# Kernel optimization log

Measured on AMD Instinct MI355X. Metric: run time of the kernel, lower is better.

The kernel has to match this reference:

```python
import jax, jax.numpy as jnp
import numpy as np

B, L, C, K, S = 8, 4096, 512, 5, 8


def setup_inputs() -> dict:
    key = jax.random.key(0)
    ks = jax.random.split(key, 5)
    x = jax.random.normal(ks[0], (B, L, C), dtype=jnp.float32)
    # contiguous random partition of [0, L) into S segments per batch row
    rng = np.random.default_rng(0)
    cuts = np.sort(rng.integers(1, L, size=(B, S - 1)), axis=1)
    starts = np.concatenate([np.zeros((B, 1), np.int64), cuts.astype(np.int64)], axis=1)
    ends = np.concatenate([cuts.astype(np.int64), np.full((B, 1), L, np.int64)], axis=1)
    segment_boundaries = jnp.asarray(np.stack([starts, ends], axis=-1))  # [B,S,2]
    fan = 1.0 / np.sqrt(K)
    w_dw = jax.random.normal(ks[1], (C, K), dtype=jnp.float32) * fan
    b_dw = jax.random.normal(ks[2], (C,), dtype=jnp.float32) * 0.01
    w_pw = jax.random.normal(ks[3], (C, C), dtype=jnp.float32) * (1.0 / np.sqrt(C))
    b_pw = jax.random.normal(ks[4], (C,), dtype=jnp.float32) * 0.01
    return {"x": x, "segment_boundaries": segment_boundaries,
            "w_dw": w_dw, "b_dw": b_dw, "w_pw": w_pw, "b_pw": b_pw}


def reference(x, segment_boundaries, w_dw, b_dw, w_pw, b_pw):
    # x: [B,L,C]; segment_boundaries: [B,S,2]; w_dw: [C,K]; w_pw: [C_out,C_in]
    Bx, Lx, Cx = x.shape
    Kx = w_dw.shape[1]
    starts = segment_boundaries[..., 0]  # [B,S]
    ends = segment_boundaries[..., 1]    # [B,S]
    pos = jnp.arange(Lx)
    in_seg = (pos[None, None, :] >= starts[..., None]) & (pos[None, None, :] < ends[..., None])  # [B,S,L]
    covered = in_seg.any(axis=1)                                  # [B,L]
    seg_id = jnp.where(covered, jnp.argmax(in_seg, axis=1), -1)   # [B,L]

    # causal depthwise conv with left zero-pad per segment (no cross-segment leakage)
    acc = jnp.zeros_like(x)
    for d in range(Kx):  # d = how far back we look; tap index = K-1-d
        if d == 0:
            x_s, id_s = x, seg_id
        else:
            x_s = jnp.pad(x, ((0, 0), (d, 0), (0, 0)))[:, :Lx]
            id_s = jnp.pad(seg_id, ((0, 0), (d, 0)), constant_values=-2)[:, :Lx]
        m = ((seg_id == id_s) & covered).astype(x.dtype)          # [B,L]
        acc = acc + w_dw[:, Kx - 1 - d] * x_s * m[..., None]
    dw = acc + b_dw                                               # [B,L,C]
    pw = jnp.einsum('blc,dc->bld', dw, w_pw) + b_pw               # pointwise 1x1 conv
    return pw * covered[..., None].astype(x.dtype)                # zeros outside segments
```

## Files before the change

kernel.cpp:

```cpp
#include <hip/hip_runtime.h>
#include <hip/hip_bf16.h>
#include <climits>

typedef __bf16 bf16;
typedef __bf16 bf16x4 __attribute__((ext_vector_type(4)));
typedef __bf16 bf16x8 __attribute__((ext_vector_type(8)));
typedef float f32x4 __attribute__((ext_vector_type(4)));

#define NB 8
#define L_ 4096
#define C_ 512
#define KW 5
#define NS 8
#define BM 64

#define BARRIER_MEM                                                            \
  do {                                                                         \
    __builtin_amdgcn_sched_barrier(0);                                         \
    __builtin_amdgcn_s_barrier();                                              \
    __builtin_amdgcn_sched_barrier(0);                                         \
  } while (0)
#define DSFLUSH_BARRIER                                                        \
  do {                                                                         \
    asm volatile("s_waitcnt lgkmcnt(0)" ::: "memory");                         \
    BARRIER_MEM;                                                               \
  } while (0)

__global__ __launch_bounds__(256) void prep_kernel(
    const float* __restrict__ w_pw, const float* __restrict__ b_dw,
    const float* __restrict__ b_pw, bf16* __restrict__ pk,
    float* __restrict__ bias2) {
  const int t = threadIdx.x;
  if (blockIdx.x < 128) {
    const int gid = blockIdx.x * 256 + t;
    const int lane = gid & 63;
    const int nf = (gid >> 6) & 3;
    const int wnn = (gid >> 8) & 7;
    const int kk = gid >> 11;
    const int n = wnn * 64 + nf * 16 + (lane & 15);
    const int c = kk * 32 + (lane >> 4) * 8;
    const float* s = w_pw + n * C_ + c;
    float4 a = *(const float4*)s;
    float4 b4 = *(const float4*)(s + 4);
    bf16x8 h;
    h[0] = (bf16)a.x; h[1] = (bf16)a.y; h[2] = (bf16)a.z; h[3] = (bf16)a.w;
    h[4] = (bf16)b4.x; h[5] = (bf16)b4.y; h[6] = (bf16)b4.z; h[7] = (bf16)b4.w;
    *(bf16x8*)(pk + (size_t)gid * 8) = h;
  } else {
    const int n = blockIdx.x - 128;
    float2 v = *(const float2*)(w_pw + n * C_ + 2 * t);
    float2 bb = *(const float2*)(b_dw + 2 * t);
    float s = v.x * bb.x + v.y * bb.y;
#pragma unroll
    for (int off = 32; off; off >>= 1) s += __shfl_down(s, off, 64);
    __shared__ float part[4];
    if ((t & 63) == 0) part[t >> 6] = s;
    __syncthreads();
    if (t == 0) bias2[n] = b_pw[n] + part[0] + part[1] + part[2] + part[3];
  }
}

__global__ __launch_bounds__(512, 2) void fused_kernel(
    const float* __restrict__ x, const int* __restrict__ segb,
    const float* __restrict__ w_dw, const bf16* __restrict__ pk,
    const float* __restrict__ bias2, float* __restrict__ out) {
  __shared__ __align__(16) bf16 As[2][BM * C_];

  const int t = threadIdx.x;
  const int lane = t & 63;
  const int b = blockIdx.x >> 5;
  const int l0 = (blockIdx.x & 31) << 7;

  const f32x4 z4 = (f32x4){0.f, 0.f, 0.f, 0.f};
  const int q = t & 127;
  const int r0 = (t >> 7) << 4;

  float4 raw[5];
#pragma unroll
  for (int i = 0; i < 5; ++i)
    raw[i] = *(const float4*)(w_dw + q * 20 + i * 4);
  f32x4 wt[5];
#pragma unroll
  for (int m = 0; m < 5; ++m)
#pragma unroll
    for (int i = 0; i < 4; ++i) {
      const int f = i * 5 + m;
      wt[m][i] = ((const float*)&raw[f >> 2])[f & 3];
    }
  const int* sb = segb + b * NS * 2;
  int stv[NS];
#pragma unroll
  for (int s = 0; s < NS; ++s) stv[s] = sb[2 * s];
  auto nxt = [&](int l) {
    int nn = INT_MAX;
#pragma unroll
    for (int s = 0; s < NS; ++s)
      nn = (stv[s] > l && stv[s] < nn) ? stv[s] : nn;
    return nn;
  };

  f32x4 w0 = z4, w1 = z4, w2 = z4, w3 = z4;
  int ns = 0;

  auto dorow = [&](bf16* dst, int l, f32x4& A, f32x4& B4, f32x4& Cc, f32x4& D,
                   const f32x4& E, int rloc) {
    if (l == ns) { A = z4; B4 = z4; Cc = z4; D = z4; ns = nxt(l); }
    f32x4 r;
#pragma unroll
    for (int i = 0; i < 4; ++i) {
      float a = A[i] * wt[0][i];
      a = fmaf(B4[i], wt[1][i], a);
      a = fmaf(Cc[i], wt[2][i], a);
      a = fmaf(D[i], wt[3][i], a);
      a = fmaf(E[i], wt[4][i], a);
      r[i] = a;
    }
    bf16x4 h;
#pragma unroll
    for (int i = 0; i < 4; ++i) h[i] = (bf16)r[i];
    const int u = q ^ ((rloc & 7) << 1);
    *(bf16x4*)&dst[rloc * 512 + u * 4] = h;
  };

  {
    ns = nxt(l0 + r0 - 4);
    const float* gxb = x + (size_t)(b * L_ + l0 + r0) * C_ + q * 4;
    f32x4 p0[4], p1[4], p2[4];
    auto ldg = [&](int g, f32x4 (&p)[4]) {
#pragma unroll
      for (int j = 0; j < 4; ++j)
        p[j] = *(const f32x4*)(gxb + (ptrdiff_t)(g * 4 + j) * C_);
    };
    ldg(0, p0);
    ldg(1, p1);
    ldg(2, p2);
#pragma unroll
    for (int i = 0; i < 4; ++i) {
      const int l = l0 + r0 - 4 + i;
      f32x4 nv = z4;
      if (l >= 0) nv = *(const f32x4*)(gxb + (ptrdiff_t)(i - 4) * C_);
      if (l == ns) { w0 = z4; w1 = z4; w2 = z4; w3 = z4; ns = nxt(l); }
      w0 = w1; w1 = w2; w2 = w3; w3 = nv;
    }
    auto compute = [&](int g, f32x4 (&p)[4]) {
      const int lb = l0 + r0 + g * 4;
      const int rl = r0 + g * 4;
      dorow((bf16*)As[0], lb + 0, w0, w1, w2, w3, p[0], rl + 0);
      dorow((bf16*)As[0], lb + 1, w1, w2, w3, p[0], p[1], rl + 1);
      dorow((bf16*)As[0], lb + 2, w2, w3, p[0], p[1], p[2], rl + 2);
      dorow((bf16*)As[0], lb + 3, w3, p[0], p[1], p[2], p[3], rl + 3);
      w0 = p[0]; w1 = p[1]; w2 = p[2]; w3 = p[3];
    };
    compute(0, p0);
    ldg(3, p0);
    compute(1, p1);
    compute(2, p2);
    compute(3, p0);
  }
  DSFLUSH_BARRIER;

  const int wn = t >> 6;
  const int cg = lane >> 4;
  const int rx = lane & 7;
  int aRow[4];
#pragma unroll
  for (int mf = 0; mf < 4; ++mf) aRow[mf] = (mf * 16 + (lane & 15)) * 512;
  const bf16* pw = pk + (size_t)wn * 2048 + lane * 8;

  f32x4 acc[4][4];
#pragma unroll
  for (int i = 0; i < 4; ++i)
#pragma unroll
    for (int j = 0; j < 4; ++j) acc[i][j] = z4;

  auto gemm_step = [&](const bf16* Ab, int kk) {
    const bf16* pws = pw + kk * 16384;
    bf16x8 bb[4];
#pragma unroll
    for (int nf = 0; nf < 4; ++nf)
      bb[nf] = *(const bf16x8*)(pws + nf * 512);
    const int ao = ((kk * 4 + cg) ^ rx) << 3;
    bf16x8 af[4];
#pragma unroll
    for (int mf = 0; mf < 4; ++mf)
      af[mf] = *(const bf16x8*)&Ab[aRow[mf] + ao];
    __builtin_amdgcn_s_setprio(1);
#pragma unroll
    for (int nf = 0; nf < 4; ++nf)
#pragma unroll
      for (int mf = 0; mf < 4; ++mf)
        acc[mf][nf] = __builtin_amdgcn_mfma_f32_16x16x32_bf16(
            af[mf], bb[nf], acc[mf][nf], 0, 0, 0);
    __builtin_amdgcn_s_setprio(0);
  };

  auto epilogue = [&](int tileOff) {
    const int col0 = wn * 64 + (lane & 15);
    float bia[4];
#pragma unroll
    for (int nf = 0; nf < 4; ++nf) bia[nf] = bias2[col0 + nf * 16];
    const int rb0 = l0 + tileOff + (cg << 2);
#pragma unroll
    for (int mf = 0; mf < 4; ++mf) {
#pragma unroll
      for (int i = 0; i < 4; ++i) {
        const int row = rb0 + mf * 16 + i;
        float* o = out + (size_t)(b * L_ + row) * C_ + col0;
#pragma unroll
        for (int nf = 0; nf < 4; ++nf) o[nf * 16] = acc[mf][nf][i] + bia[nf];
      }
    }
  };

  {
    ns = nxt(l0 + 64 + r0 - 4);
    const float* gxb1 = x + (size_t)(b * L_ + l0 + 64 + r0) * C_ + q * 4;
    f32x4 pA[4], pB[4];
    auto ldg1 = [&](int g, f32x4 (&p)[4]) {
#pragma unroll
      for (int j = 0; j < 4; ++j)
        p[j] = *(const f32x4*)(gxb1 + (ptrdiff_t)(g * 4 + j) * C_);
    };
    {
      f32x4 hw[4];
#pragma unroll
      for (int i = 0; i < 4; ++i)
        hw[i] = *(const f32x4*)(gxb1 + (ptrdiff_t)(i - 4) * C_);
      ldg1(0, pA);
      w0 = z4; w1 = z4; w2 = z4; w3 = z4;
#pragma unroll
      for (int i = 0; i < 4; ++i) {
        const int l = l0 + 64 + r0 - 4 + i;
        if (l == ns) { w0 = z4; w1 = z4; w2 = z4; w3 = z4; ns = nxt(l); }
        w0 = w1; w1 = w2; w2 = w3; w3 = hw[i];
      }
    }
    auto convg = [&](int g, f32x4 (&p)[4]) {
      const int lb = l0 + 64 + r0 + g * 4;
      const int rl = r0 + g * 4;
      dorow((bf16*)As[1], lb + 0, w0, w1, w2, w3, p[0], rl + 0);
      dorow((bf16*)As[1], lb + 1, w1, w2, w3, p[0], p[1], rl + 1);
      dorow((bf16*)As[1], lb + 2, w2, w3, p[0], p[1], p[2], rl + 2);
      dorow((bf16*)As[1], lb + 3, w3, p[0], p[1], p[2], p[3], rl + 3);
      w0 = p[0]; w1 = p[1]; w2 = p[2]; w3 = p[3];
    };
    const bf16* A0 = (const bf16*)As[0];
    ldg1(1, pB);
    convg(0, pA);
    gemm_step(A0, 0); gemm_step(A0, 1); gemm_step(A0, 2); gemm_step(A0, 3);
    ldg1(2, pA);
    convg(1, pB);
    gemm_step(A0, 4); gemm_step(A0, 5); gemm_step(A0, 6); gemm_step(A0, 7);
    ldg1(3, pB);
    convg(2, pA);
    gemm_step(A0, 8); gemm_step(A0, 9); gemm_step(A0, 10); gemm_step(A0, 11);
    convg(3, pB);
    gemm_step(A0, 12); gemm_step(A0, 13); gemm_step(A0, 14); gemm_step(A0, 15);
  }

  epilogue(0);

  DSFLUSH_BARRIER;

#pragma unroll
  for (int i = 0; i < 4; ++i)
#pragma unroll
    for (int j = 0; j < 4; ++j) acc[i][j] = z4;
  {
    const bf16* A1 = (const bf16*)As[1];
#pragma unroll 1
    for (int kk = 0; kk < 16; ++kk) gemm_step(A1, kk);
  }
  epilogue(64);
}

extern "C" void kernel_launch(void* const* d_in, const int* in_sizes, int n_in,
                              void* d_out, int out_size, void* d_ws,
                              size_t ws_size, hipStream_t stream) {
  const float* x = (const float*)d_in[0];
  const int* segb = (const int*)d_in[1];
  const float* w_dw = (const float*)d_in[2];
  const float* b_dw = (const float*)d_in[3];
  const float* w_pw = (const float*)d_in[4];
  const float* b_pw = (const float*)d_in[5];
  float* out = (float*)d_out;

  float* bias2 = (float*)d_ws;
  bf16* pk = (bf16*)((char*)d_ws + 4096);

  prep_kernel<<<640, 256, 0, stream>>>(w_pw, b_dw, b_pw, pk, bias2);
  fused_kernel<<<NB * L_ / 128, 512, 0, stream>>>(x, segb, w_dw, pk, bias2,
                                                  out);
}
```

Baseline: 43.25 us.

## Double block size to 1024 threads, halving per-thread conv and GEMM work

Raises the fused kernel's block size from 512 to 1024 threads. The depthwise conv now handles 2 channels per thread instead of 4, and the GEMM uses a 2x8 wave grid, so each wave covers 32 rows instead of 64. The aim is more waves in flight per CU and lower register pressure to better hide memory latency. The cost is smaller per-thread loads (8-byte instead of 16-byte), repeated B-operand global loads across the two row-halves of waves, and heavier barrier participation. The launch bounds hint of 4 blocks of 1024 threads may not be achievable, given that each block uses 128KB of LDS.

```diff
diff --git a/kernel.cpp b/kernel.cpp
--- a/kernel.cpp
+++ b/kernel.cpp
@@ -3,8 +3,9 @@
 #include <climits>
 
 typedef __bf16 bf16;
-typedef __bf16 bf16x4 __attribute__((ext_vector_type(4)));
+typedef __bf16 bf16x2 __attribute__((ext_vector_type(2)));
 typedef __bf16 bf16x8 __attribute__((ext_vector_type(8)));
+typedef float f32x2 __attribute__((ext_vector_type(2)));
 typedef float f32x4 __attribute__((ext_vector_type(4)));
 
 #define NB 8
@@ -60,7 +61,7 @@
   }
 }
 
-__global__ __launch_bounds__(512, 2) void fused_kernel(
+__global__ __launch_bounds__(1024, 4) void fused_kernel(
     const float* __restrict__ x, const int* __restrict__ segb,
     const float* __restrict__ w_dw, const bf16* __restrict__ pk,
     const float* __restrict__ bias2, float* __restrict__ out) {
@@ -68,25 +69,25 @@
 
   const int t = threadIdx.x;
   const int lane = t & 63;
+  const int wid = t >> 6;
   const int b = blockIdx.x >> 5;
   const int l0 = (blockIdx.x & 31) << 7;
 
-  const f32x4 z4 = (f32x4){0.f, 0.f, 0.f, 0.f};
-  const int q = t & 127;
-  const int r0 = (t >> 7) << 4;
-
-  float4 raw[5];
+  const f32x2 z2 = (f32x2){0.f, 0.f};
+  const int q2 = t & 255;
+  const int r0 = (t >> 8) << 4;
+
+  float e[10];
 #pragma unroll
   for (int i = 0; i < 5; ++i)
-    raw[i] = *(const float4*)(w_dw + q * 20 + i * 4);
-  f32x4 wt[5];
-#pragma unroll
-  for (int m = 0; m < 5; ++m)
-#pragma unroll
-    for (int i = 0; i < 4; ++i) {
-      const int f = i * 5 + m;
-      wt[m][i] = ((const float*)&raw[f >> 2])[f & 3];
-    }
+    *(float2*)(e + 2 * i) = *(const float2*)(w_dw + q2 * 10 + 2 * i);
+  f32x2 wt[5];
+#pragma unroll
+  for (int m = 0; m < 5; ++m) {
+    wt[m][0] = e[m];
+    wt[m][1] = e[5 + m];
+  }
+
   const int* sb = segb + b * NS * 2;
   int stv[NS];
 #pragma unroll
@@ -99,15 +100,15 @@
     return nn;
   };
 
-  f32x4 w0 = z4, w1 = z4, w2 = z4, w3 = z4;
+  f32x2 w0 = z2, w1 = z2, w2 = z2, w3 = z2;
   int ns = 0;
 
-  auto dorow = [&](bf16* dst, int l, f32x4& A, f32x4& B4, f32x4& Cc, f32x4& D,
-                   const f32x4& E, int rloc) {
-    if (l == ns) { A = z4; B4 = z4; Cc = z4; D = z4; ns = nxt(l); }
-    f32x4 r;
-#pragma unroll
-    for (int i = 0; i < 4; ++i) {
+  auto dorow = [&](bf16* dst, int l, f32x2& A, f32x2& B4, f32x2& Cc, f32x2& D,
+                   const f32x2& E, int rloc) {
+    if (l == ns) { A = z2; B4 = z2; Cc = z2; D = z2; ns = nxt(l); }
+    f32x2 r;
+#pragma unroll
+    for (int i = 0; i < 2; ++i) {
       float a = A[i] * wt[0][i];
       a = fmaf(B4[i], wt[1][i], a);
       a = fmaf(Cc[i], wt[2][i], a);
@@ -115,21 +116,21 @@
       a = fmaf(E[i], wt[4][i], a);
       r[i] = a;
     }
-    bf16x4 h;
-#pragma unroll
-    for (int i = 0; i < 4; ++i) h[i] = (bf16)r[i];
-    const int u = q ^ ((rloc & 7) << 1);
-    *(bf16x4*)&dst[rloc * 512 + u * 4] = h;
+    bf16x2 h;
+    h[0] = (bf16)r[0];
+    h[1] = (bf16)r[1];
+    const int u = q2 ^ ((rloc & 7) << 2);
+    *(bf16x2*)&dst[rloc * 512 + u * 2] = h;
   };
 
   {
     ns = nxt(l0 + r0 - 4);
-    const float* gxb = x + (size_t)(b * L_ + l0 + r0) * C_ + q * 4;
-    f32x4 p0[4], p1[4], p2[4];
-    auto ldg = [&](int g, f32x4 (&p)[4]) {
+    const float* gxb = x + (size_t)(b * L_ + l0 + r0) * C_ + q2 * 2;
+    f32x2 p0[4], p1[4], p2[4];
+    auto ldg = [&](int g, f32x2 (&p)[4]) {
 #pragma unroll
       for (int j = 0; j < 4; ++j)
-        p[j] = *(const f32x4*)(gxb + (ptrdiff_t)(g * 4 + j) * C_);
+        p[j] = *(const f32x2*)(gxb + (ptrdiff_t)(g * 4 + j) * C_);
     };
     ldg(0, p0);
     ldg(1, p1);
@@ -137,12 +138,12 @@
 #pragma unroll
     for (int i = 0; i < 4; ++i) {
       const int l = l0 + r0 - 4 + i;
-      f32x4 nv = z4;
-      if (l >= 0) nv = *(const f32x4*)(gxb + (ptrdiff_t)(i - 4) * C_);
-      if (l == ns) { w0 = z4; w1 = z4; w2 = z4; w3 = z4; ns = nxt(l); }
+      f32x2 nv = z2;
+      if (l >= 0) nv = *(const f32x2*)(gxb + (ptrdiff_t)(i - 4) * C_);
+      if (l == ns) { w0 = z2; w1 = z2; w2 = z2; w3 = z2; ns = nxt(l); }
       w0 = w1; w1 = w2; w2 = w3; w3 = nv;
     }
-    auto compute = [&](int g, f32x4 (&p)[4]) {
+    auto compute = [&](int g, f32x2 (&p)[4]) {
       const int lb = l0 + r0 + g * 4;
       const int rl = r0 + g * 4;
       dorow((bf16*)As[0], lb + 0, w0, w1, w2, w3, p[0], rl + 0);
@@ -159,19 +160,22 @@
   }
   DSFLUSH_BARRIER;
 
-  const int wn = t >> 6;
+  const int wm = wid >> 3;
+  const int wn = wid & 7;
   const int cg = lane >> 4;
   const int rx = lane & 7;
-  int aRow[4];
-#pragma unroll
-  for (int mf = 0; mf < 4; ++mf) aRow[mf] = (mf * 16 + (lane & 15)) * 512;
+
+  int aRow[2];
+#pragma unroll
+  for (int mf = 0; mf < 2; ++mf)
+    aRow[mf] = (wm * 32 + mf * 16 + (lane & 15)) * 512;
   const bf16* pw = pk + (size_t)wn * 2048 + lane * 8;
 
-  f32x4 acc[4][4];
-#pragma unroll
-  for (int i = 0; i < 4; ++i)
-#pragma unroll
-    for (int j = 0; j < 4; ++j) acc[i][j] = z4;
+  f32x4 acc[2][4];
+#pragma unroll
+  for (int i = 0; i < 2; ++i)
+#pragma unroll
+    for (int j = 0; j < 4; ++j) acc[i][j] = (f32x4){0.f, 0.f, 0.f, 0.f};
 
   auto gemm_step = [&](const bf16* Ab, int kk) {
     const bf16* pws = pw + kk * 16384;
@@ -180,15 +184,15 @@
     for (int nf = 0; nf < 4; ++nf)
       bb[nf] = *(const bf16x8*)(pws + nf * 512);
     const int ao = ((kk * 4 + cg) ^ rx) << 3;
-    bf16x8 af[4];
-#pragma unroll
-    for (int mf = 0; mf < 4; ++mf)
+    bf16x8 af[2];
+#pragma unroll
+    for (int mf = 0; mf < 2; ++mf)
       af[mf] = *(const bf16x8*)&Ab[aRow[mf] + ao];
     __builtin_amdgcn_s_setprio(1);
 #pragma unroll
     for (int nf = 0; nf < 4; ++nf)
 #pragma unroll
-      for (int mf = 0; mf < 4; ++mf)
+      for (int mf = 0; mf < 2; ++mf)
         acc[mf][nf] = __builtin_amdgcn_mfma_f32_16x16x32_bf16(
             af[mf], bb[nf], acc[mf][nf], 0, 0, 0);
     __builtin_amdgcn_s_setprio(0);
@@ -199,9 +203,9 @@
     float bia[4];
 #pragma unroll
     for (int nf = 0; nf < 4; ++nf) bia[nf] = bias2[col0 + nf * 16];
-    const int rb0 = l0 + tileOff + (cg << 2);
-#pragma unroll
-    for (int mf = 0; mf < 4; ++mf) {
+    const int rb0 = l0 + tileOff + wm * 32 + (cg << 2);
+#pragma unroll
+    for (int mf = 0; mf < 2; ++mf) {
 #pragma unroll
       for (int i = 0; i < 4; ++i) {
         const int row = rb0 + mf * 16 + i;
@@ -214,28 +218,28 @@
 
   {
     ns = nxt(l0 + 64 + r0 - 4);
-    const float* gxb1 = x + (size_t)(b * L_ + l0 + 64 + r0) * C_ + q * 4;
-    f32x4 pA[4], pB[4];
-    auto ldg1 = [&](int g, f32x4 (&p)[4]) {
+    const float* gxb1 = x + (size_t)(b * L_ + l0 + 64 + r0) * C_ + q2 * 2;
+    f32x2 pA[4], pB[4];
+    auto ldg1 = [&](int g, f32x2 (&p)[4]) {
 #pragma unroll
       for (int j = 0; j < 4; ++j)
-        p[j] = *(const f32x4*)(gxb1 + (ptrdiff_t)(g * 4 + j) * C_);
+        p[j] = *(const f32x2*)(gxb1 + (ptrdiff_t)(g * 4 + j) * C_);
     };
     {
-      f32x4 hw[4];
+      f32x2 hw[4];
 #pragma unroll
       for (int i = 0; i < 4; ++i)
-        hw[i] = *(const f32x4*)(gxb1 + (ptrdiff_t)(i - 4) * C_);
+        hw[i] = *(const f32x2*)(gxb1 + (ptrdiff_t)(i - 4) * C_);
       ldg1(0, pA);
-      w0 = z4; w1 = z4; w2 = z4; w3 = z4;
+      w0 = z2; w1 = z2; w2 = z2; w3 = z2;
 #pragma unroll
       for (int i = 0; i < 4; ++i) {
         const int l = l0 + 64 + r0 - 4 + i;
-        if (l == ns) { w0 = z4; w1 = z4; w2 = z4; w3 = z4; ns = nxt(l); }
+        if (l == ns) { w0 = z2; w1 = z2; w2 = z2; w3 = z2; ns = nxt(l); }
         w0 = w1; w1 = w2; w2 = w3; w3 = hw[i];
       }
     }
-    auto convg = [&](int g, f32x4 (&p)[4]) {
+    auto convg = [&](int g, f32x2 (&p)[4]) {
       const int lb = l0 + 64 + r0 + g * 4;
       const int rl = r0 + g * 4;
       dorow((bf16*)As[1], lb + 0, w0, w1, w2, w3, p[0], rl + 0);
@@ -263,9 +267,9 @@
   DSFLUSH_BARRIER;
 
 #pragma unroll
-  for (int i = 0; i < 4; ++i)
-#pragma unroll
-    for (int j = 0; j < 4; ++j) acc[i][j] = z4;
+  for (int i = 0; i < 2; ++i)
+#pragma unroll
+    for (int j = 0; j < 4; ++j) acc[i][j] = (f32x4){0.f, 0.f, 0.f, 0.f};
   {
     const bf16* A1 = (const bf16*)As[1];
 #pragma unroll 1
@@ -289,6 +293,6 @@
   bf16* pk = (bf16*)((char*)d_ws + 4096);
 
   prep_kernel<<<640, 256, 0, stream>>>(w_pw, b_dw, b_pw, pk, bias2);
-  fused_kernel<<<NB * L_ / 128, 512, 0, stream>>>(x, segb, w_dw, pk, bias2,
-                                                  out);
+  fused_kernel<<<NB * L_ / 128, 1024, 0, stream>>>(x, segb, w_dw, pk, bias2,
+                                                   out);
 }
```

Result: slower. 47.09 us (+8.9%).
